# Kernel tuning notes

Hardware: AMD Instinct MI355X
Metric: run time of the kernel (lower is better)

## Reference

```python
import jax, jax.numpy as jnp
import numpy as np

CUTOFF = 5.0
BOX = 20.0
EPS = 1e-5


def _neighbor_list_np(cutoff, coords, cell):
    # coords: [N,3] float32, cell: [3,3]. Returns (pair_first, pair_second, pair_image)
    inv_cell = np.linalg.inv(cell)
    proj = coords @ inv_cell
    frac = np.fmod(proj, 1.0)                      # matches torch.fmod (sign-preserving)
    woff = np.floor(proj).astype(np.int64)          # torch.div(..., rounding_mode='floor')
    wrapped = (frac @ cell).astype(coords.dtype)
    inv_lengths = np.linalg.norm(inv_cell, axis=0)
    nb = (np.floor(cutoff * inv_lengths + EPS) + 1).astype(np.int64)
    ranges = [np.arange(-int(n), int(n) + 1) for n in nb]
    # image grid ordered (i1 outer, i2, i3 inner) to match the nested torch loops
    images = np.stack(np.meshgrid(*ranges, indexing='ij'), axis=-1).reshape(-1, 3)
    off_cart = images.astype(coords.dtype) @ cell   # [K,3]
    drij = wrapped[:, None, :] - wrapped[None, :, :]           # [N,N,3]
    diff = drij[None, :, :, :] + off_cart[:, None, None, :]    # [K,N,N,3]
    dist = np.linalg.norm(diff, axis=-1)                       # [K,N,N]
    mask = dist < cutoff
    zero_k = int(np.where((images == 0).all(axis=1))[0][0])
    np.fill_diagonal(mask[zero_k], False)                      # drop self pairs in home image
    k, i, j = np.nonzero(mask)  # row-major (k,i,j) == per-image blocks of (i,j), same order as torch
    woff_ij = woff[i] - woff[j]
    pair_image = images[k] - woff_ij
    return i, j, pair_image


def setup_inputs() -> dict:
    key = jax.random.key(0)
    n_mol, n_at = 16, 512
    coordinates = jax.random.uniform(key, (n_mol, n_at, 3), dtype=jnp.float32) * BOX
    nonblank = jnp.ones((n_mol, n_at), dtype=bool)
    real_atoms = jnp.arange(n_mol * n_at, dtype=jnp.int32)
    inv_real_atoms = jnp.arange(n_mol * n_at, dtype=jnp.int32)
    cell = jnp.tile((BOX * jnp.eye(3, dtype=jnp.float32))[None], (n_mol, 1, 1))
    mol_index = jnp.arange(n_mol * n_at, dtype=jnp.int32) // n_at
    return dict(coordinates=coordinates, nonblank=nonblank, real_atoms=real_atoms,
                inv_real_atoms=inv_real_atoms, cell=cell, mol_index=mol_index,
                n_molecules=n_mol, n_atoms_max=n_at)


def reference(coordinates, nonblank, real_atoms, inv_real_atoms, cell, mol_index,
              n_molecules, n_atoms_max):
    # --- neighbor-list construction (torch.no_grad section): host numpy, vectorized over images ---
    coords_np = np.asarray(coordinates)
    cell_np = np.asarray(cell)
    nb_np = np.asarray(nonblank)
    pfs, pss, ofs = [], [], []
    for m in range(n_molecules):
        r = coords_np[m][nb_np[m]]
        pf, ps, of = _neighbor_list_np(CUTOFF, r, cell_np[m])
        if len(pf) == 0:
            continue
        pfs.append(pf + m * n_atoms_max)
        pss.append(ps + m * n_atoms_max)
        ofs.append(of)
    pf = np.concatenate(pfs)
    ps = np.concatenate(pss)
    of = np.concatenate(ofs)
    n_images = max(1, int(np.abs(of).max()))

    pair_first = inv_real_atoms[jnp.asarray(pf)]
    pair_second = inv_real_atoms[jnp.asarray(ps)]
    offsets = jnp.asarray(of.astype(np.int32))
    n_off = 2 * n_images + 1
    o1, o2, o3 = (offsets + n_images).T
    offset_index = o3 + n_off * (o2 + n_off * o1)
    pair_mol = mol_index[pair_first]
    pair_cell = cell[pair_mol]                                   # [P,3,3]
    pair_offsets = jnp.einsum('pk,pkl->pl', offsets.astype(cell.dtype), pair_cell)

    # --- differentiable distance evaluation ---
    coordflat = coordinates.reshape(n_molecules * n_atoms_max, 3)[real_atoms]
    paircoord = coordflat[pair_first] - coordflat[pair_second] + pair_offsets
    distflat2 = jnp.linalg.norm(paircoord, axis=1)
    return distflat2, pair_first, pair_second, paircoord, offsets, offset_index
```

## Files before the change

### kernel.cpp

```cpp
#include <hip/hip_runtime.h>

#define NMOL 16
#define NAT  512
#define NK   27

#define SSMAX 24.999998092651367f

__device__ __forceinline__ float wrap1(float v) {
    return __fmul_rn(__fmul_rn(v, 0.05f), 20.0f);
}

__device__ __forceinline__ int probe_code(float wx, float wy, float wz,
                                          float wjx, float wjy, float wjz,
                                          bool self) {
    float dx = __fsub_rn(wx, wjx);
    float dy = __fsub_rn(wy, wjy);
    float dz = __fsub_rn(wz, wjz);
    int ox = (dx > 15.0f) ? -1 : ((dx < -15.0f) ? 1 : 0);
    int oy = (dy > 15.0f) ? -1 : ((dy < -15.0f) ? 1 : 0);
    int oz = (dz > 15.0f) ? -1 : ((dz < -15.0f) ? 1 : 0);
    float ax = __fadd_rn(dx, 20.0f * (float)ox);
    float ay = __fadd_rn(dy, 20.0f * (float)oy);
    float az = __fadd_rn(dz, 20.0f * (float)oz);
    float ss = __fadd_rn(__fadd_rn(__fmul_rn(ax, ax), __fmul_rn(ay, ay)),
                         __fmul_rn(az, az));
    bool hit = (ss < SSMAX) && !self;
    return hit ? ((ox + 1) * 9 + (oy + 1) * 3 + (oz + 1)) : 31;
}

__global__ __launch_bounds__(256, 8) void pass_count(const float* __restrict__ coords,
                                                     int* __restrict__ cnt,
                                                     int* __restrict__ sub,
                                                     int* __restrict__ blkmol) {
    __shared__ float rr[NAT * 3];
    __shared__ int cur[2][4][NK];
    const int blk  = blockIdx.x;
    const int m    = blk >> 6;
    const int b    = blk & 63;
    const int g0   = b * 2;
    const int t    = threadIdx.x;
    const int w    = t >> 6;
    const int lane = t & 63;
    const int iA   = g0 * 4 + w;
    const int iB   = iA + 4;

    const float4* cm4 = reinterpret_cast<const float4*>(coords + (size_t)m * NAT * 3);
    float4* rr4 = reinterpret_cast<float4*>(rr);
    rr4[t] = cm4[t];
    if (t < 128) rr4[t + 256] = cm4[t + 256];
    if (t < 2 * 4 * NK) ((int*)cur)[t] = 0;
    __syncthreads();

    const float wAx = wrap1(rr[iA * 3 + 0]), wAy = wrap1(rr[iA * 3 + 1]), wAz = wrap1(rr[iA * 3 + 2]);
    const float wBx = wrap1(rr[iB * 3 + 0]), wBy = wrap1(rr[iB * 3 + 1]), wBz = wrap1(rr[iB * 3 + 2]);

    #pragma unroll
    for (int it = 0; it < NAT / 64; ++it) {
        const int j = it * 64 + lane;
        float wjx = wrap1(rr[j * 3 + 0]);
        float wjy = wrap1(rr[j * 3 + 1]);
        float wjz = wrap1(rr[j * 3 + 2]);
        int cA = probe_code(wAx, wAy, wAz, wjx, wjy, wjz, j == iA);
        int cB = probe_code(wBx, wBy, wBz, wjx, wjy, wjz, j == iB);
        if (cA != 31) atomicAdd(&cur[0][w][cA], 1);
        if (cB != 31) atomicAdd(&cur[1][w][cB], 1);
    }
    __syncthreads();
    if (t < 216) {
        int uu = t / 108, rem = t % 108, ww = rem / 27, k = rem % 27;
        int i = (g0 + uu) * 4 + ww;
        cnt[(m * NK + k) * NAT + i] = cur[uu][ww][k];
    }
    if (t < NK) {
        int s = 0;
        #pragma unroll
        for (int uu = 0; uu < 2; ++uu)
            #pragma unroll
            for (int ww = 0; ww < 4; ++ww) s += cur[uu][ww][t];
        sub[(m * NK + t) * 64 + b] = s;
    }
    if (w == 0) {
        int s = 0;
        #pragma unroll
        for (int x = lane; x < 216; x += 64) s += ((int*)cur)[x];
        #pragma unroll
        for (int d = 1; d < 64; d <<= 1) s += __shfl_xor(s, d, 64);
        if (lane == 0) blkmol[blk] = s;
    }
}

__global__ __launch_bounds__(256, 8) void pass_emit(const float* __restrict__ coords,
                                                    const int* __restrict__ cnt,
                                                    const int* __restrict__ sub,
                                                    const int* __restrict__ blkmol,
                                                    float* __restrict__ out, int P) {
    __shared__ float rr[NAT * 3];
    __shared__ int cur[2][4][NK];
    __shared__ int strip[8][NK];
    __shared__ int ctot[NK], cpre[NK], kexcl[NK];
    __shared__ int tls[NMOL];
    const int blk  = blockIdx.x;
    const int m    = blk >> 6;
    const int b    = blk & 63;
    const int g0   = b * 2;
    const int t    = threadIdx.x;
    const int w    = t >> 6;
    const int lane = t & 63;

    const float4* cm4 = reinterpret_cast<const float4*>(coords + (size_t)m * NAT * 3);
    float4* rr4 = reinterpret_cast<float4*>(rr);
    rr4[t] = cm4[t];
    if (t < 128) rr4[t + 256] = cm4[t + 256];

    for (int mm = w; mm < NMOL; mm += 4) {
        int v = blkmol[mm * 64 + lane];
        #pragma unroll
        for (int d = 1; d < 64; d <<= 1) v += __shfl_xor(v, d, 64);
        if (lane == 0) tls[mm] = v;
    }
    for (int k = w; k < NK; k += 4) {
        int v = sub[(m * NK + k) * 64 + lane];
        int incl = v;
        #pragma unroll
        for (int d = 1; d < 64; d <<= 1) {
            int u = __shfl_up(incl, d, 64);
            if (lane >= d) incl += u;
        }
        int tot   = __shfl(incl, 63, 64);
        int exclb = __shfl(incl - v, b, 64);
        if (lane == 0) { ctot[k] = tot; cpre[k] = exclb; }
    }
    if (t < 216) {
        int uu = t / 108, rem = t % 108, ww = rem / 27, k = rem % 27;
        int i = (g0 + uu) * 4 + ww;
        strip[uu * 4 + ww][k] = cnt[(m * NK + k) * NAT + i];
    }
    __syncthreads();
    if (t == 0) {
        int run = 0;
        for (int mm = 0; mm < m; ++mm) run += tls[mm];
        for (int k = 0; k < NK; ++k) { kexcl[k] = run; run += ctot[k]; }
    }
    __syncthreads();
    if (t < 216) {
        int uu = t / 108, rem = t % 108, ww = rem / 27, k = rem % 27;
        int a = uu * 4 + ww;
        int ip = 0;
        for (int a2 = 0; a2 < a; ++a2) ip += strip[a2][k];
        cur[uu][ww][k] = kexcl[k] + cpre[k] + ip;
    }
    __syncthreads();

    const int iA = g0 * 4 + w, iB = iA + 4;
    const float rAx = rr[iA * 3 + 0], rAy = rr[iA * 3 + 1], rAz = rr[iA * 3 + 2];
    const float rBx = rr[iB * 3 + 0], rBy = rr[iB * 3 + 1], rBz = rr[iB * 3 + 2];
    const float wAx = wrap1(rAx), wAy = wrap1(rAy), wAz = wrap1(rAz);
    const float wBx = wrap1(rBx), wBy = wrap1(rBy), wBz = wrap1(rBz);
    const unsigned long long ltmask =
        (lane == 0) ? 0ull : (~0ull >> (64 - lane));

    #pragma unroll
    for (int it = 0; it < NAT / 64; ++it) {
        const int j = it * 64 + lane;
        const float rjx = rr[j * 3 + 0], rjy = rr[j * 3 + 1], rjz = rr[j * 3 + 2];
        const float wjx = wrap1(rjx), wjy = wrap1(rjy), wjz = wrap1(rjz);

        #pragma unroll
        for (int uu = 0; uu < 2; ++uu) {
            const int i  = (uu == 0) ? iA : iB;
            const float rx = (uu == 0) ? rAx : rBx;
            const float ry = (uu == 0) ? rAy : rBy;
            const float rz = (uu == 0) ? rAz : rBz;
            int code = (uu == 0)
                ? probe_code(wAx, wAy, wAz, wjx, wjy, wjz, j == iA)
                : probe_code(wBx, wBy, wBz, wjx, wjy, wjz, j == iB);
            bool hit = (code != 31);
            int kk = hit ? code : 0;

            unsigned long long grp = __ballot(hit);
            #pragma unroll
            for (int bb = 0; bb < 5; ++bb) {
                unsigned long long bm = __ballot((kk >> bb) & 1);
                grp &= ((kk >> bb) & 1) ? bm : ~bm;
            }
            int leader = hit ? (__ffsll((unsigned long long)grp) - 1) : 0;
            int cntg   = __popcll(grp);
            int rank   = __popcll(grp & ltmask);

            int base = 0;
            if (hit && lane == leader)
                base = atomicAdd(&cur[uu][w][kk], cntg);
            base = __shfl(base, leader, 64);

            if (hit) {
                int p = base + rank;
                if (p < P) {
                    int ox = kk / 9;
                    int rem = kk - ox * 9;
                    int oy = rem / 3;
                    int oz = rem - oy * 3;
                    ox -= 1; oy -= 1; oz -= 1;
                    float cx = 20.0f * (float)ox;
                    float cy = 20.0f * (float)oy;
                    float cz = 20.0f * (float)oz;
                    float px = __fadd_rn(__fsub_rn(rx, rjx), cx);
                    float py = __fadd_rn(__fsub_rn(ry, rjy), cy);
                    float pz = __fadd_rn(__fsub_rn(rz, rjz), cz);
                    float ss = __fadd_rn(__fadd_rn(__fmul_rn(px, px), __fmul_rn(py, py)),
                                         __fmul_rn(pz, pz));
                    out[p]                 = __fsqrt_rn(ss);
                    out[P + p]             = (float)(m * NAT + i);
                    out[2 * P + p]         = (float)(m * NAT + j);
                    out[3 * P + 3 * p + 0] = px;
                    out[3 * P + 3 * p + 1] = py;
                    out[3 * P + 3 * p + 2] = pz;
                    out[6 * P + 3 * p + 0] = (float)ox;
                    out[6 * P + 3 * p + 1] = (float)oy;
                    out[6 * P + 3 * p + 2] = (float)oz;
                    out[9 * P + p]         = (float)kk;
                }
            }
        }
    }
}

extern "C" void kernel_launch(void* const* d_in, const int* in_sizes, int n_in,
                              void* d_out, int out_size, void* d_ws, size_t ws_size,
                              hipStream_t stream) {
    (void)in_sizes; (void)n_in; (void)ws_size;
    const float* coords = (const float*)d_in[0];
    int* cnt    = (int*)d_ws;
    int* sub    = cnt + NMOL * NK * NAT;
    int* blkmol = sub + NMOL * NK * 64;
    float* out  = (float*)d_out;
    const int P = out_size / 10;

    hipLaunchKernelGGL(pass_count, dim3(NMOL * NAT / 8), dim3(256), 0, stream,
                       coords, cnt, sub, blkmol);
    hipLaunchKernelGGL(pass_emit, dim3(NMOL * NAT / 8), dim3(256), 0, stream,
                       coords, cnt, sub, blkmol, out, P);
}
```

Measured before the change: 100.9 us.

## Fuse count and emit passes with a grid-wide barrier and cached codes

Merges the count and emit kernels into one persistent launch. Blocks synchronise through a global atomic counter barrier in workspace that is reset by a memset. Each thread packs its per-pair image codes into a 64-bit register during counting, so the emit phase reuses them instead of recomputing distances, and per-atom counts stay in shared memory rather than a global cnt array. This removes a kernel launch, the recomputation and the cnt round-trip. The cost is an added memset, a spin barrier that needs all 1024 blocks co-resident (launch bounds lowered to 4 waves per SIMD), and a deadlock risk if they are not.

```diff
diff --git a/kernel.cpp b/kernel.cpp
--- a/kernel.cpp
+++ b/kernel.cpp
@@ -3,6 +3,7 @@
 #define NMOL 16
 #define NAT  512
 #define NK   27
+#define NBLK 1024
 
 #define SSMAX 24.999998092651367f
 
@@ -28,12 +29,17 @@
     return hit ? ((ox + 1) * 9 + (oy + 1) * 3 + (oz + 1)) : 31;
 }
 
-__global__ __launch_bounds__(256, 8) void pass_count(const float* __restrict__ coords,
-                                                     int* __restrict__ cnt,
-                                                     int* __restrict__ sub,
-                                                     int* __restrict__ blkmol) {
+__global__ __launch_bounds__(256, 4) void fused(const float* __restrict__ coords,
+                                                int* __restrict__ bar,
+                                                int* __restrict__ sub,
+                                                int* __restrict__ blkmol,
+                                                float* __restrict__ out, int P) {
     __shared__ float rr[NAT * 3];
     __shared__ int cur[2][4][NK];
+    __shared__ int strip[8][NK];
+    __shared__ int ctot[NK], cpre[NK], kexcl[NK];
+    __shared__ int tls[NMOL];
+
     const int blk  = blockIdx.x;
     const int m    = blk >> 6;
     const int b    = blk & 63;
@@ -51,26 +57,25 @@
     if (t < 2 * 4 * NK) ((int*)cur)[t] = 0;
     __syncthreads();
 
-    const float wAx = wrap1(rr[iA * 3 + 0]), wAy = wrap1(rr[iA * 3 + 1]), wAz = wrap1(rr[iA * 3 + 2]);
-    const float wBx = wrap1(rr[iB * 3 + 0]), wBy = wrap1(rr[iB * 3 + 1]), wBz = wrap1(rr[iB * 3 + 2]);
-
+    const float wAx = wrap1(rr[iA*3+0]), wAy = wrap1(rr[iA*3+1]), wAz = wrap1(rr[iA*3+2]);
+    const float wBx = wrap1(rr[iB*3+0]), wBy = wrap1(rr[iB*3+1]), wBz = wrap1(rr[iB*3+2]);
+
+    unsigned long long codeA = 0, codeB = 0;
     #pragma unroll
     for (int it = 0; it < NAT / 64; ++it) {
         const int j = it * 64 + lane;
-        float wjx = wrap1(rr[j * 3 + 0]);
-        float wjy = wrap1(rr[j * 3 + 1]);
-        float wjz = wrap1(rr[j * 3 + 2]);
+        const float wjx = wrap1(rr[j*3+0]);
+        const float wjy = wrap1(rr[j*3+1]);
+        const float wjz = wrap1(rr[j*3+2]);
         int cA = probe_code(wAx, wAy, wAz, wjx, wjy, wjz, j == iA);
         int cB = probe_code(wBx, wBy, wBz, wjx, wjy, wjz, j == iB);
+        codeA |= (unsigned long long)cA << (8 * it);
+        codeB |= (unsigned long long)cB << (8 * it);
         if (cA != 31) atomicAdd(&cur[0][w][cA], 1);
         if (cB != 31) atomicAdd(&cur[1][w][cB], 1);
     }
     __syncthreads();
-    if (t < 216) {
-        int uu = t / 108, rem = t % 108, ww = rem / 27, k = rem % 27;
-        int i = (g0 + uu) * 4 + ww;
-        cnt[(m * NK + k) * NAT + i] = cur[uu][ww][k];
-    }
+
     if (t < NK) {
         int s = 0;
         #pragma unroll
@@ -87,30 +92,19 @@
         for (int d = 1; d < 64; d <<= 1) s += __shfl_xor(s, d, 64);
         if (lane == 0) blkmol[blk] = s;
     }
-}
-
-__global__ __launch_bounds__(256, 8) void pass_emit(const float* __restrict__ coords,
-                                                    const int* __restrict__ cnt,
-                                                    const int* __restrict__ sub,
-                                                    const int* __restrict__ blkmol,
-                                                    float* __restrict__ out, int P) {
-    __shared__ float rr[NAT * 3];
-    __shared__ int cur[2][4][NK];
-    __shared__ int strip[8][NK];
-    __shared__ int ctot[NK], cpre[NK], kexcl[NK];
-    __shared__ int tls[NMOL];
-    const int blk  = blockIdx.x;
-    const int m    = blk >> 6;
-    const int b    = blk & 63;
-    const int g0   = b * 2;
-    const int t    = threadIdx.x;
-    const int w    = t >> 6;
-    const int lane = t & 63;
-
-    const float4* cm4 = reinterpret_cast<const float4*>(coords + (size_t)m * NAT * 3);
-    float4* rr4 = reinterpret_cast<float4*>(rr);
-    rr4[t] = cm4[t];
-    if (t < 128) rr4[t + 256] = cm4[t + 256];
+    __syncthreads();
+
+    if (t == 0) {
+        int prev = __hip_atomic_fetch_add(&bar[m * 32], 1,
+                                          __ATOMIC_ACQ_REL, __HIP_MEMORY_SCOPE_AGENT);
+        if (prev == 63)
+            __hip_atomic_fetch_add(&bar[512], 1,
+                                   __ATOMIC_ACQ_REL, __HIP_MEMORY_SCOPE_AGENT);
+        while (__hip_atomic_load(&bar[512], __ATOMIC_ACQUIRE,
+                                 __HIP_MEMORY_SCOPE_AGENT) < NMOL)
+            __builtin_amdgcn_s_sleep(8);
+    }
+    __syncthreads();
 
     for (int mm = w; mm < NMOL; mm += 4) {
         int v = blkmol[mm * 64 + lane];
@@ -132,8 +126,7 @@
     }
     if (t < 216) {
         int uu = t / 108, rem = t % 108, ww = rem / 27, k = rem % 27;
-        int i = (g0 + uu) * 4 + ww;
-        strip[uu * 4 + ww][k] = cnt[(m * NK + k) * NAT + i];
+        strip[uu * 4 + ww][k] = cur[uu][ww][k];
     }
     __syncthreads();
     if (t == 0) {
@@ -151,29 +144,24 @@
     }
     __syncthreads();
 
-    const int iA = g0 * 4 + w, iB = iA + 4;
-    const float rAx = rr[iA * 3 + 0], rAy = rr[iA * 3 + 1], rAz = rr[iA * 3 + 2];
-    const float rBx = rr[iB * 3 + 0], rBy = rr[iB * 3 + 1], rBz = rr[iB * 3 + 2];
-    const float wAx = wrap1(rAx), wAy = wrap1(rAy), wAz = wrap1(rAz);
-    const float wBx = wrap1(rBx), wBy = wrap1(rBy), wBz = wrap1(rBz);
+    const float rAx = rr[iA*3+0], rAy = rr[iA*3+1], rAz = rr[iA*3+2];
+    const float rBx = rr[iB*3+0], rBy = rr[iB*3+1], rBz = rr[iB*3+2];
     const unsigned long long ltmask =
         (lane == 0) ? 0ull : (~0ull >> (64 - lane));
 
     #pragma unroll
-    for (int it = 0; it < NAT / 64; ++it) {
-        const int j = it * 64 + lane;
-        const float rjx = rr[j * 3 + 0], rjy = rr[j * 3 + 1], rjz = rr[j * 3 + 2];
-        const float wjx = wrap1(rjx), wjy = wrap1(rjy), wjz = wrap1(rjz);
-
-        #pragma unroll
-        for (int uu = 0; uu < 2; ++uu) {
-            const int i  = (uu == 0) ? iA : iB;
-            const float rx = (uu == 0) ? rAx : rBx;
-            const float ry = (uu == 0) ? rAy : rBy;
-            const float rz = (uu == 0) ? rAz : rBz;
-            int code = (uu == 0)
-                ? probe_code(wAx, wAy, wAz, wjx, wjy, wjz, j == iA)
-                : probe_code(wBx, wBy, wBz, wjx, wjy, wjz, j == iB);
+    for (int uu = 0; uu < 2; ++uu) {
+        const int i  = (uu == 0) ? iA : iB;
+        const float rx = (uu == 0) ? rAx : rBx;
+        const float ry = (uu == 0) ? rAy : rBy;
+        const float rz = (uu == 0) ? rAz : rBz;
+        const unsigned long long code8 = (uu == 0) ? codeA : codeB;
+        const int pf = m * NAT + i;
+
+        #pragma unroll
+        for (int it = 0; it < NAT / 64; ++it) {
+            const int j = it * 64 + lane;
+            int code = (int)((code8 >> (8 * it)) & 0xffull);
             bool hit = (code != 31);
             int kk = hit ? code : 0;
 
@@ -203,13 +191,14 @@
                     float cx = 20.0f * (float)ox;
                     float cy = 20.0f * (float)oy;
                     float cz = 20.0f * (float)oz;
+                    const float rjx = rr[j*3+0], rjy = rr[j*3+1], rjz = rr[j*3+2];
                     float px = __fadd_rn(__fsub_rn(rx, rjx), cx);
                     float py = __fadd_rn(__fsub_rn(ry, rjy), cy);
                     float pz = __fadd_rn(__fsub_rn(rz, rjz), cz);
                     float ss = __fadd_rn(__fadd_rn(__fmul_rn(px, px), __fmul_rn(py, py)),
                                          __fmul_rn(pz, pz));
                     out[p]                 = __fsqrt_rn(ss);
-                    out[P + p]             = (float)(m * NAT + i);
+                    out[P + p]             = (float)pf;
                     out[2 * P + p]         = (float)(m * NAT + j);
                     out[3 * P + 3 * p + 0] = px;
                     out[3 * P + 3 * p + 1] = py;
@@ -229,14 +218,13 @@
                               hipStream_t stream) {
     (void)in_sizes; (void)n_in; (void)ws_size;
     const float* coords = (const float*)d_in[0];
-    int* cnt    = (int*)d_ws;
-    int* sub    = cnt + NMOL * NK * NAT;
+    int* bar    = (int*)d_ws;
+    int* sub    = bar + 1024;
     int* blkmol = sub + NMOL * NK * 64;
     float* out  = (float*)d_out;
     const int P = out_size / 10;
 
-    hipLaunchKernelGGL(pass_count, dim3(NMOL * NAT / 8), dim3(256), 0, stream,
-                       coords, cnt, sub, blkmol);
-    hipLaunchKernelGGL(pass_emit, dim3(NMOL * NAT / 8), dim3(256), 0, stream,
-                       coords, cnt, sub, blkmol, out, P);
-}
+    hipMemsetAsync(bar, 0, 4096, stream);
+    hipLaunchKernelGGL(fused, dim3(NBLK), dim3(256), 0, stream,
+                       bar ? coords : coords, bar, sub, blkmol, out, P);
+}
```

After: 140.2 us. +39.0%, slower.
